# Optimization experiments

Hardware: AMD Instinct MI355X
Metric: run time of the kernel (lower is better)

The kernel has to match this reference:

```python
import jax, jax.numpy as jnp
import numpy as np

B, C, N, K, G = 4, 128, 4096, 9, 4


def setup_inputs() -> dict:
    key = jax.random.key(0)
    ks = jax.random.split(key, 4)
    s = 0.05
    return {
        "features": jax.random.normal(ks[0], (B, C, N, 1), jnp.float32),
        # Attn.linear: Conv2d(2C -> C, 1x1)
        "w_lin": jax.random.normal(ks[1], (C, 2 * C), jnp.float32) * s,
        "b_lin": jnp.zeros((C,), jnp.float32),
        # atten_weight_conv: Linear(C -> K*G)
        "w_aw": jax.random.normal(ks[2], (K * G, C), jnp.float32) * s,
        "b_aw": jnp.zeros((K * G,), jnp.float32),
        # GroupNorm(4, C)
        "gn_g": jnp.ones((C,), jnp.float32),
        "gn_b": jnp.zeros((C,), jnp.float32),
        # conv: Conv2d(C -> C, 1x1) + BatchNorm2d(C)
        "conv_w": jax.random.normal(ks[3], (C, C), jnp.float32) * s,
        "conv_b": jnp.zeros((C,), jnp.float32),
        "bn_g": jnp.ones((C,), jnp.float32),
        "bn_b": jnp.zeros((C,), jnp.float32),
    }


def reference(features, w_lin, b_lin, w_aw, b_aw, gn_g, gn_b, conv_w, conv_b, bn_g, bn_b):
    B, C, N, _ = features.shape
    K, G = 9, 4
    Cg = C // G  # 32 channels per group
    EPS = 1e-5

    x = features[..., 0]                       # [B,C,N]
    # ---- KNN graph (negative squared distance, top-k) ----
    xx = jnp.sum(x * x, axis=1)                # [B,N]
    inner = jnp.einsum('bcn,bcm->bnm', x, x)   # [B,N,N]
    pd = 2.0 * inner - xx[:, :, None] - xx[:, None, :]
    idx = jax.lax.top_k(pd, K)[1]              # [B,N,K]

    # ---- edge feature gather: cat(x, x - x_neighbor) ----
    xt = x.transpose(0, 2, 1)                  # [B,N,C]
    b_ix = jnp.arange(B)[:, None, None]
    nbr = xt[b_ix, idx]                        # [B,N,K,C]
    ctr = jnp.broadcast_to(xt[:, :, None, :], (B, N, K, C))
    edge = jnp.concatenate([ctr, ctr - nbr], axis=-1)   # [B,N,K,2C]

    # ---- Attn.linear (1x1 conv == per-position linear) ----
    feat = jnp.einsum('bnke,ce->bnkc', edge, w_lin) + b_lin  # [B,N,K,C]

    # ---- grouped channel attention (4 groups of 32) ----
    fg = feat.reshape(B, N, K, G, Cg)
    scores = jnp.einsum('bnkgc,bnjgc->bngkj', fg, fg) / np.sqrt(32.0)
    s = jax.nn.softmax(scores, axis=-1)        # [B,N,G,K,K]
    attn = jnp.einsum('bngkj,bnjgc->bngkc', s, jax.nn.elu(fg))  # [B,N,G,K,Cg]

    # ---- attention weights over neighbors ----
    aw = jnp.einsum('bnc,dc->bnd', xt, w_aw) + b_aw          # [B,N,K*G]
    aw = jax.nn.softmax(aw.reshape(B, N, G, K), axis=-1)     # [B,N,G,K]

    # ---- weighted neighbor combine ----
    lf = jnp.einsum('bngk,bngkc->bngc', aw, attn)            # [B,N,G,Cg]
    lf = lf.transpose(0, 2, 3, 1).reshape(B, C, N, 1)        # [B,C,N,1]

    # ---- GroupNorm(4, C) over residual ----
    y = lf + features
    yg = y.reshape(B, G, Cg * N)
    mu = yg.mean(-1, keepdims=True)
    var = yg.var(-1, keepdims=True)
    yn = ((yg - mu) / jnp.sqrt(var + EPS)).reshape(B, C, N, 1)
    yn = yn * gn_g[None, :, None, None] + gn_b[None, :, None, None]

    # ---- 1x1 conv + BatchNorm (training-mode batch stats) + ReLU ----
    z = jnp.einsum('oc,bcnk->bonk', conv_w, yn) + conv_b[None, :, None, None]
    m = z.mean(axis=(0, 2, 3), keepdims=True)
    v = z.var(axis=(0, 2, 3), keepdims=True)
    z = (z - m) / jnp.sqrt(v + EPS) * bn_g[None, :, None, None] + bn_b[None, :, None, None]
    return jax.nn.relu(z)
```

## Files before the change

### kernel.cpp

```cpp
#include <hip/hip_runtime.h>
#include <hip/hip_bf16.h>
#include <cstddef>

#define NPTS 4096
#define CCH  128
#define KNN  9
#define GRP  4
#define BB   4
#define OFF_XT    0u
#define OFF_XX    2097152u
#define OFF_XHI   2113536u
#define OFF_IDX   3162112u
#define OFF_O     3309568u
#define OFF_Y     8159232u
#define OFF_GNP   10256384u
#define OFF_GNA   10387456u
#define OFF_GND   10387968u
#define OFF_WP    10388480u
#define OFF_BIASP 10454016u
#define OFF_BNSUM 10454528u
#define OFF_BNSQ  10454656u
#define OFF_BNSC  10454784u
#define OFF_BNSH  10454912u

using bf16x8 = __attribute__((ext_vector_type(8))) short;
using f32x4  = __attribute__((ext_vector_type(4))) float;

#define CE(a, b) { float _h = fmaxf(a, b); b = fminf(a, b); a = _h; }

#define SENT_BITS 0xFF7FF000u

__global__ void k_transpose(const float* __restrict__ x, float* __restrict__ xt,
                            __hip_bfloat16* __restrict__ xhi, float* __restrict__ xx) {
  __shared__ float t[32][33];
  int tx = threadIdx.x, ty = threadIdx.y;
  int n0 = blockIdx.x * 32, c0 = blockIdx.y * 32, b = blockIdx.z;
  float v = x[((size_t)b * CCH + c0 + ty) * NPTS + n0 + tx];
  t[ty][tx] = v;
  __syncthreads();
  float tv = t[tx][ty];
  size_t R = (size_t)b * NPTS + n0 + ty;
  int c = c0 + tx;
  xt[R * CCH + c] = tv;
  int g = c >> 3, w = c & 7;
  int sc = (((g ^ ((n0 + ty) & 15)) << 3) | w);
  xhi[R * CCH + sc] = __float2bfloat16(tv);
  if (ty == 0) {
    float s = 0.f;
    #pragma unroll
    for (int k = 0; k < 32; k++) { float u = t[k][tx]; s += u * u; }
    atomicAdd(&xx[b * NPTS + n0 + tx], s);
  }
}

__device__ __forceinline__ void select_chunk(int c, int wave, int quad,
                                             const f32x4 (&acc)[2][2],
                                             float (&top8)[2][8]) {
  const unsigned cbase = (unsigned)(c * 128 + wave * 32 + quad * 4);
  #pragma unroll
  for (int qt = 0; qt < 2; qt++) {
    float k[8];
    #pragma unroll
    for (int ct = 0; ct < 2; ct++)
      #pragma unroll
      for (int r = 0; r < 4; r++) {
        unsigned u = __float_as_uint(acc[ct][qt][r]);
        k[ct * 4 + r] = __uint_as_float((u & 0xFFFFF000u) |
                                        (cbase + (unsigned)(ct * 16 + r)));
      }
    CE(k[0],k[1]) CE(k[2],k[3]) CE(k[4],k[5]) CE(k[6],k[7])
    CE(k[0],k[2]) CE(k[1],k[3]) CE(k[4],k[6]) CE(k[5],k[7])
    CE(k[1],k[2]) CE(k[5],k[6])
    CE(k[0],k[4]) CE(k[1],k[5]) CE(k[2],k[6]) CE(k[3],k[7])
    CE(k[2],k[4]) CE(k[3],k[5])
    CE(k[1],k[2]) CE(k[3],k[4]) CE(k[5],k[6])
    float t[8];
    #pragma unroll
    for (int i = 0; i < 8; i++) t[i] = fmaxf(top8[qt][i], k[7 - i]);
    CE(t[0],t[4]) CE(t[1],t[5]) CE(t[2],t[6]) CE(t[3],t[7])
    CE(t[0],t[2]) CE(t[1],t[3]) CE(t[4],t[6]) CE(t[5],t[7])
    CE(t[0],t[1]) CE(t[2],t[3]) CE(t[4],t[5]) CE(t[6],t[7])
    #pragma unroll
    for (int i = 0; i < 8; i++) top8[qt][i] = t[i];
  }
}

__device__ __forceinline__ void load_chunk(const short* __restrict__ xb,
                                           const int (&aoff)[2][4], int c,
                                           bf16x8 (&af)[2][4]) {
  const short* cb = xb + c * (128 * CCH);
  #pragma unroll
  for (int ct = 0; ct < 2; ct++)
    #pragma unroll
    for (int ks = 0; ks < 4; ks++)
      af[ct][ks] = *(const bf16x8*)(cb + aoff[ct][ks]);
}

__launch_bounds__(256, 3)
__global__ void k_knn(const short* __restrict__ xhi, const float* __restrict__ xx,
                      float* __restrict__ cand) {
  __shared__ short Qs[32 * 136];
  __shared__ float XXs[2048];
  const int tid = threadIdx.x;
  const int wave = tid >> 6, lane = tid & 63;
  const int quad = lane >> 4, m = lane & 15;
  const int b = blockIdx.y;
  const int q0 = blockIdx.x * 32;
  const int ch0 = blockIdx.z * 16;
  const short* xb = xhi + (size_t)b * NPTS * CCH;
  const float* xxb = xx + (b << 12);

  {
    int f = tid;
    #pragma unroll
    for (int it = 0; it < 2; it++, f += 256) {
      int row = f >> 4, s = f & 15;
      bf16x8 v = *(const bf16x8*)(xb + (size_t)(q0 + row) * CCH + s * 8);
      int g = s ^ (row & 15);
      *(bf16x8*)&Qs[row * 136 + g * 8] = v;
    }
    const float4* src4 = (const float4*)(xxb + ch0 * 128);
    float4* dst4 = (float4*)XXs;
    #pragma unroll
    for (int j = 0; j < 2; j++) {
      float4 v = src4[tid * 2 + j];
      dst4[tid * 2 + j] = make_float4(-0.5f * v.x, -0.5f * v.y, -0.5f * v.z, -0.5f * v.w);
    }
  }

  int aoff[2][4];
  #pragma unroll
  for (int ct = 0; ct < 2; ct++)
    #pragma unroll
    for (int ks = 0; ks < 4; ks++)
      aoff[ct][ks] = (wave * 32 + ct * 16 + m) * CCH + (((ks * 4 + quad) ^ m) * 8);

  float top8[2][8];
  #pragma unroll
  for (int qt = 0; qt < 2; qt++)
    #pragma unroll
    for (int p = 0; p < 8; p++) top8[qt][p] = __uint_as_float(SENT_BITS);

  f32x4 acc[2][2];
  bf16x8 bufA[2][4], bufB[2][4];

  unsigned qoff = (unsigned)(m * 272 + quad * 16);
  const unsigned xbase = (unsigned)(wave * 128 + quad * 16);

  load_chunk(xb, aoff, ch0, bufA);
  __syncthreads();

  auto mfma_lds = [&](const bf16x8 (&af)[2][4], int crel) {
    unsigned xo = xbase + (unsigned)crel * 512u;
    f32x4 ci0 = *(const f32x4*)((const char*)XXs + xo);
    f32x4 ci1 = *(const f32x4*)((const char*)XXs + xo + 64);
    acc[0][0] = ci0; acc[0][1] = ci0; acc[1][0] = ci1; acc[1][1] = ci1;
    #pragma unroll
    for (int ks = 0; ks < 4; ks++) {
      bf16x8 qv0 = *(const bf16x8*)((const char*)Qs + qoff + ks * 64);
      bf16x8 qv1 = *(const bf16x8*)((const char*)Qs + qoff + 4352 + ks * 64);
      acc[0][0] = __builtin_amdgcn_mfma_f32_16x16x32_bf16(af[0][ks], qv0, acc[0][0], 0, 0, 0);
      acc[0][1] = __builtin_amdgcn_mfma_f32_16x16x32_bf16(af[0][ks], qv1, acc[0][1], 0, 0, 0);
      acc[1][0] = __builtin_amdgcn_mfma_f32_16x16x32_bf16(af[1][ks], qv0, acc[1][0], 0, 0, 0);
      acc[1][1] = __builtin_amdgcn_mfma_f32_16x16x32_bf16(af[1][ks], qv1, acc[1][1], 0, 0, 0);
    }
  };

  for (int c = ch0; c < ch0 + 16; c += 2) {
    load_chunk(xb, aoff, c + 1, bufB);
    if (c > ch0) select_chunk(c - 1, wave, quad, acc, top8);
    asm volatile("" : "+v"(qoff));
    mfma_lds(bufA, c - ch0);
    if (c + 2 < ch0 + 16) load_chunk(xb, aoff, c + 2, bufA);
    select_chunk(c, wave, quad, acc, top8);
    asm volatile("" : "+v"(qoff));
    mfma_lds(bufB, c + 1 - ch0);
  }
  select_chunk(ch0 + 15, wave, quad, acc, top8);

  int slot = wave * 4 + quad;
  #pragma unroll
  for (int qt = 0; qt < 2; qt++) {
    int q = q0 + qt * 16 + m;
    float* dst = cand + ((size_t)((b << 12) + q) * 32 + blockIdx.z * 16 + slot) * 8;
    #pragma unroll
    for (int p = 0; p < 8; p++) dst[p] = top8[qt][p];
  }
}

__launch_bounds__(256)
__global__ void k_rerank(const float* __restrict__ cand, const float* __restrict__ xt,
                         const float* __restrict__ xx, int* __restrict__ idxOut) {
  __shared__ __align__(16) float arr[4][128];
  __shared__ int selS[4][16];
  __shared__ float keyS[4][16];
  int tid = threadIdx.x, wave = tid >> 6, lane = tid & 63;
  int qg = blockIdx.x * 4 + wave;
  int b = qg >> 12;
  const float* src = cand + (size_t)qg * 256;
  if (lane < 16) {
    float4 a0 = *(const float4*)&src[lane * 8];
    float4 a1 = *(const float4*)&src[lane * 8 + 4];
    float4 b0 = *(const float4*)&src[128 + lane * 8];
    float4 b1 = *(const float4*)&src[128 + lane * 8 + 4];
    arr[wave][lane * 8 + 0] = fmaxf(a0.x, b1.w);
    arr[wave][lane * 8 + 1] = fmaxf(a0.y, b1.z);
    arr[wave][lane * 8 + 2] = fmaxf(a0.z, b1.y);
    arr[wave][lane * 8 + 3] = fmaxf(a0.w, b1.x);
    arr[wave][lane * 8 + 4] = fmaxf(a1.x, b0.w);
    arr[wave][lane * 8 + 5] = fmaxf(a1.y, b0.z);
    arr[wave][lane * 8 + 6] = fmaxf(a1.z, b0.y);
    arr[wave][lane * 8 + 7] = fmaxf(a1.w, b0.x);
  }
  __syncthreads();
  float e1 = arr[wave][lane], e2 = arr[wave][lane + 64];
  int r1 = 0, r2 = 0;
  #pragma unroll 8
  for (int f = 0; f < 128; f += 4) {
    float4 fv = *(const float4*)&arr[wave][f];
    r1 += (fv.x > e1) + (fv.y > e1) + (fv.z > e1) + (fv.w > e1);
    r2 += (fv.x > e2) + (fv.y > e2) + (fv.z > e2) + (fv.w > e2);
  }
  if (r1 < 16) selS[wave][r1] = (int)(__float_as_uint(e1) & 0xFFFu);
  if (r2 < 16) selS[wave][r2] = (int)(__float_as_uint(e2) & 0xFFFu);
  __syncthreads();
  int cnum = lane >> 2, part = lane & 3;
  int cidx = selS[wave][cnum];
  const float* rq = xt + (size_t)qg * CCH;
  const float* rc = xt + ((size_t)(b << 12) + cidx) * CCH;
  float dot = 0.f;
  #pragma unroll
  for (int j = 0; j < 8; j++) {
    float4 a4 = *(const float4*)&rq[part * 32 + j * 4];
    float4 c4 = *(const float4*)&rc[part * 32 + j * 4];
    dot += a4.x * c4.x + a4.y * c4.y + a4.z * c4.z + a4.w * c4.w;
  }
  dot += __shfl_xor(dot, 1);
  dot += __shfl_xor(dot, 2);
  if (part == 0)
    keyS[wave][cnum] = fmaf(2.f, dot, -xx[(b << 12) + cidx]);
  __syncthreads();
  if (lane < 16) {
    float k = keyS[wave][lane]; int i = selS[wave][lane];
    int r = 0;
    #pragma unroll
    for (int f = 0; f < 16; f++) {
      float fk = keyS[wave][f]; int fi = selS[wave][f];
      r += (fk > k) || (fk == k && fi < i);
    }
    if (r < 9) idxOut[(size_t)qg * 9 + r] = i;
  }
}

__launch_bounds__(256)
__global__ void k_linear(const float* __restrict__ xt, const float* __restrict__ w_lin,
                         const float* __restrict__ b_lin, const float* __restrict__ w_aw,
                         const float* __restrict__ b_aw, float* __restrict__ O) {
  __shared__ __align__(16) float Xs[64 * 132];
  __shared__ __align__(16) float Ws[64 * 132];
  int tid = threadIdx.x;
  int tx = tid & 15, ty = tid >> 4;
  int p0 = blockIdx.x * 64, o0 = blockIdx.y * 64;
  #pragma unroll
  for (int i = 0; i < 8; i++) {
    int flat = tid + i * 256; int r = flat >> 5, c4 = flat & 31;
    *(float4*)&Xs[r * 132 + c4 * 4] = *(const float4*)&xt[(size_t)(p0 + r) * CCH + c4 * 4];
  }
  #pragma unroll
  for (int i = 0; i < 8; i++) {
    int flat = tid + i * 256; int r = flat >> 5, c4 = flat & 31;
    int o = o0 + r; float4 v;
    if (o < 128) {
      float4 a = *(const float4*)&w_lin[(size_t)o * 256 + c4 * 4];
      float4 c = *(const float4*)&w_lin[(size_t)o * 256 + 128 + c4 * 4];
      v = make_float4(a.x + c.x, a.y + c.y, a.z + c.z, a.w + c.w);
    } else if (o < 256) {
      v = *(const float4*)&w_lin[(size_t)(o - 128) * 256 + 128 + c4 * 4];
    } else if (o < 292) {
      v = *(const float4*)&w_aw[(size_t)(o - 256) * 128 + c4 * 4];
    } else v = make_float4(0.f, 0.f, 0.f, 0.f);
    *(float4*)&Ws[r * 132 + c4 * 4] = v;
  }
  __syncthreads();
  float acc[4][4] = {};
  #pragma unroll 2
  for (int kq = 0; kq < 32; kq++) {
    float4 xa[4], wb[4];
    #pragma unroll
    for (int i = 0; i < 4; i++) xa[i] = *(const float4*)&Xs[(ty * 4 + i) * 132 + kq * 4];
    #pragma unroll
    for (int j = 0; j < 4; j++) wb[j] = *(const float4*)&Ws[(tx + 16 * j) * 132 + kq * 4];
    #pragma unroll
    for (int i = 0; i < 4; i++)
      #pragma unroll
      for (int j = 0; j < 4; j++)
        acc[i][j] += xa[i].x * wb[j].x + xa[i].y * wb[j].y + xa[i].z * wb[j].z + xa[i].w * wb[j].w;
  }
  #pragma unroll
  for (int j = 0; j < 4; j++) {
    int o = o0 + tx + 16 * j;
    if (o < 292) {
      float bias = (o < 128) ? b_lin[o] : ((o < 256) ? 0.f : b_aw[o - 256]);
      #pragma unroll
      for (int i = 0; i < 4; i++)
        O[(size_t)(p0 + ty * 4 + i) * 296 + o] = acc[i][j] + bias;
    }
  }
}

__launch_bounds__(256)
__global__ void k_attn(const float* __restrict__ O, const int* __restrict__ idxArr,
                       const float* __restrict__ xt, float* __restrict__ Y,
                       float* __restrict__ gnPart) {
  __shared__ __align__(16) float fF[4][1188];
  __shared__ __align__(16) float scS[4][432];
  __shared__ float awS[4][48];
  __shared__ float w9S[4][48];
  __shared__ int tI[45], tJ[45];
  int tid = threadIdx.x;
  int wave = tid >> 6, l = tid & 63;
  int pos = blockIdx.x * 4 + wave;
  int b = pos >> 12;
  if (tid == 0) {
    int p = 0;
    for (int i = 0; i < 9; i++) for (int j = i; j < 9; j++) { tI[p] = i; tJ[p] = j; p++; }
  }
  int nbr[9];
  const float* Op = O + (size_t)pos * 296;
  #pragma unroll
  for (int k = 0; k < 9; k++) nbr[k] = idxArr[(size_t)pos * 9 + k];
  float2 u = *(const float2*)(Op + 2 * l);
  float* fFw = fF[wave];
  #pragma unroll
  for (int k = 0; k < 9; k++) {
    const float* vp = O + (size_t)((b << 12) + nbr[k]) * 296 + 128;
    float2 vv = *(const float2*)(vp + 2 * l);
    *(float2*)&fFw[k * 132 + 2 * l] = make_float2(u.x - vv.x, u.y - vv.y);
  }
  __syncthreads();
  #pragma unroll
  for (int r = 0; r < 3; r++) {
    int p = r * 64 + l;
    if (p < 180) {
      int g = p / 45, q = p - g * 45;
      int i = tI[q], j = tJ[q];
      const float* fi = fFw + i * 132 + g * 32;
      const float* fj = fFw + j * 132 + g * 32;
      float s = 0.f;
      #pragma unroll
      for (int t8 = 0; t8 < 8; t8++) {
        float4 a4 = *(const float4*)(fi + 4 * t8);
        float4 b4 = *(const float4*)(fj + 4 * t8);
        s += a4.x * b4.x + a4.y * b4.y + a4.z * b4.z + a4.w * b4.w;
      }
      s *= 0.17677669529663687f;
      scS[wave][(g * 9 + i) * 12 + j] = s;
      scS[wave][(g * 9 + j) * 12 + i] = s;
    }
  }
  __syncthreads();
  if (l < 36) {
    int g = l / 9, i = l - g * 9;
    float* rp = &scS[wave][(g * 9 + i) * 12];
    float mx = rp[0];
    #pragma unroll
    for (int j = 1; j < 9; j++) mx = fmaxf(mx, rp[j]);
    float e[9]; float sm = 0.f;
    #pragma unroll
    for (int j = 0; j < 9; j++) { e[j] = __expf(rp[j] - mx); sm += e[j]; }
    float inv = 1.f / sm;
    #pragma unroll
    for (int j = 0; j < 9; j++) rp[j] = e[j] * inv;
  } else if (l < 40) {
    int g = l - 36;
    float a[9]; float mx = -3.4e38f;
    #pragma unroll
    for (int k = 0; k < 9; k++) { a[k] = Op[256 + g * 9 + k]; mx = fmaxf(mx, a[k]); }
    float sm = 0.f;
    #pragma unroll
    for (int k = 0; k < 9; k++) { a[k] = __expf(a[k] - mx); sm += a[k]; }
    float inv = 1.f / sm;
    #pragma unroll
    for (int k = 0; k < 9; k++) awS[wave][g * 12 + k] = a[k] * inv;
  }
  __syncthreads();
  if (l < 36) {
    int g = l / 9, j = l - g * 9;
    float s = 0.f;
    #pragma unroll
    for (int i = 0; i < 9; i++) s += awS[wave][g * 12 + i] * scS[wave][(g * 9 + i) * 12 + j];
    w9S[wave][g * 12 + j] = s;
  }
  __syncthreads();
  int g = l >> 4;
  float w9r[9];
  #pragma unroll
  for (int j = 0; j < 9; j++) w9r[j] = w9S[wave][g * 12 + j];
  int c0 = 2 * l;
  float lf0 = 0.f, lf1 = 0.f;
  #pragma unroll
  for (int j = 0; j < 9; j++) {
    float2 f2 = *(const float2*)&fFw[j * 132 + c0];
    float e0 = f2.x > 0.f ? f2.x : __expf(f2.x) - 1.f;
    float e1 = f2.y > 0.f ? f2.y : __expf(f2.y) - 1.f;
    lf0 += w9r[j] * e0;
    lf1 += w9r[j] * e1;
  }
  float2 xv = *(const float2*)(xt + (size_t)pos * CCH + c0);
  float y0 = lf0 + xv.x, y1 = lf1 + xv.y;
  *(float2*)(Y + (size_t)pos * CCH + c0) = make_float2(y0, y1);
  float s1 = y0 + y1, s2 = y0 * y0 + y1 * y1;
  #pragma unroll
  for (int mm = 1; mm <= 8; mm <<= 1) { s1 += __shfl_xor(s1, mm); s2 += __shfl_xor(s2, mm); }
  if ((l & 15) == 0) {
    gnPart[(size_t)pos * 8 + g * 2]     = s1;
    gnPart[(size_t)pos * 8 + g * 2 + 1] = s2;
  }
}

__global__ void k_gnstats(const float* __restrict__ gnPart,
                          const float* __restrict__ gn_g, const float* __restrict__ gn_b,
                          float* __restrict__ gnA, float* __restrict__ gnD) {
  int bg = blockIdx.x; int b = bg >> 2, g = bg & 3;
  int tid = threadIdx.x;
  float s1 = 0.f, s2 = 0.f;
  for (int r = tid; r < NPTS; r += 256) {
    const float* p = gnPart + (size_t)(b * NPTS + r) * 8 + g * 2;
    s1 += p[0]; s2 += p[1];
  }
  __shared__ float r1[256], r2[256];
  r1[tid] = s1; r2[tid] = s2;
  __syncthreads();
  for (int off = 128; off > 0; off >>= 1) {
    if (tid < off) { r1[tid] += r1[tid + off]; r2[tid] += r2[tid + off]; }
    __syncthreads();
  }
  __shared__ float muS, rsS;
  if (tid == 0) {
    float mu = r1[0] * (1.f / 131072.f);
    float var = r2[0] * (1.f / 131072.f) - mu * mu;
    muS = mu; rsS = 1.f / sqrtf(var + 1e-5f);
  }
  __syncthreads();
  if (tid < 32) {
    int c = g * 32 + tid;
    float a = rsS * gn_g[c];
    gnA[b * 128 + c] = a;
    gnD[b * 128 + c] = gn_b[c] - muS * a;
  }
}

__global__ void k_fold(const float* __restrict__ conv_w, const float* __restrict__ conv_b,
                       const float* __restrict__ gnA, const float* __restrict__ gnD,
                       float* __restrict__ Wp, float* __restrict__ biasp) {
  int b = blockIdx.x; int tid = threadIdx.x;
  __shared__ float dS[128], aS[128];
  if (tid < 128) { dS[tid] = gnD[b * 128 + tid]; aS[tid] = gnA[b * 128 + tid]; }
  __syncthreads();
  for (int f = tid; f < 16384; f += 256)
    Wp[(size_t)b * 16384 + f] = conv_w[f] * aS[f & 127];
  if (tid < 128) {
    float s = conv_b[tid];
    for (int c = 0; c < 128; c++) s += conv_w[tid * 128 + c] * dS[c];
    biasp[b * 128 + tid] = s;
  }
}

__launch_bounds__(256)
__global__ void k_conv(const float* __restrict__ Y, const float* __restrict__ Wp,
                       const float* __restrict__ biasp, float* __restrict__ zpre,
                       float* __restrict__ bnSum, float* __restrict__ bnSq) {
  __shared__ __align__(16) float Ys[64 * 132];
  __shared__ __align__(16) float Ws[64 * 132];
  int tid = threadIdx.x;
  int tx = tid & 15, ty = tid >> 4;
  int n0 = blockIdx.x * 64, o0 = blockIdx.y * 64, b = blockIdx.z;
  #pragma unroll
  for (int i = 0; i < 8; i++) {
    int flat = tid + i * 256; int r = flat >> 5, c4 = flat & 31;
    *(float4*)&Ys[r * 132 + c4 * 4] = *(const float4*)&Y[(size_t)((b << 12) + n0 + r) * CCH + c4 * 4];
    *(float4*)&Ws[r * 132 + c4 * 4] = *(const float4*)&Wp[(size_t)b * 16384 + (size_t)(o0 + r) * 128 + c4 * 4];
  }
  __syncthreads();
  float acc[4][4] = {};
  #pragma unroll 2
  for (int kq = 0; kq < 32; kq++) {
    float4 wa[4], yb[4];
    #pragma unroll
    for (int i = 0; i < 4; i++) wa[i] = *(const float4*)&Ws[(ty * 4 + i) * 132 + kq * 4];
    #pragma unroll
    for (int j = 0; j < 4; j++) yb[j] = *(const float4*)&Ys[(tx + 16 * j) * 132 + kq * 4];
    #pragma unroll
    for (int i = 0; i < 4; i++)
      #pragma unroll
      for (int j = 0; j < 4; j++)
        acc[i][j] += wa[i].x * yb[j].x + wa[i].y * yb[j].y + wa[i].z * yb[j].z + wa[i].w * yb[j].w;
  }
  #pragma unroll
  for (int i = 0; i < 4; i++) {
    int o = o0 + ty * 4 + i;
    float bias = biasp[b * 128 + o];
    float p1 = 0.f, p2 = 0.f;
    #pragma unroll
    for (int j = 0; j < 4; j++) {
      float z = acc[i][j] + bias;
      zpre[(((size_t)((b << 7) + o)) << 12) + n0 + tx + 16 * j] = z;
      p1 += z; p2 += z * z;
    }
    #pragma unroll
    for (int mm = 1; mm <= 8; mm <<= 1) { p1 += __shfl_xor(p1, mm); p2 += __shfl_xor(p2, mm); }
    if (tx == 0) { atomicAdd(&bnSum[o], p1); atomicAdd(&bnSq[o], p2); }
  }
}

__global__ void k_bnfin(const float* __restrict__ bnSum, const float* __restrict__ bnSq,
                        const float* __restrict__ bn_g, const float* __restrict__ bn_b,
                        float* __restrict__ bnScale, float* __restrict__ bnShift) {
  int o = threadIdx.x;
  float m = bnSum[o] * (1.f / 16384.f);
  float v = bnSq[o] * (1.f / 16384.f) - m * m;
  float sc = bn_g[o] / sqrtf(v + 1e-5f);
  bnScale[o] = sc;
  bnShift[o] = bn_b[o] - m * sc;
}

__global__ void k_final(const float* __restrict__ zpre, const float* __restrict__ bnScale,
                        const float* __restrict__ bnShift, float* __restrict__ out) {
  int i4 = blockIdx.x * 256 + threadIdx.x;
  int e = i4 * 4;
  int o = (e >> 12) & 127;
  float4 z = *(const float4*)&zpre[e];
  float sc = bnScale[o], sh = bnShift[o];
  float4 r;
  r.x = fmaxf(fmaf(z.x, sc, sh), 0.f);
  r.y = fmaxf(fmaf(z.y, sc, sh), 0.f);
  r.z = fmaxf(fmaf(z.z, sc, sh), 0.f);
  r.w = fmaxf(fmaf(z.w, sc, sh), 0.f);
  *(float4*)&out[e] = r;
}

extern "C" void kernel_launch(void* const* d_in, const int* in_sizes, int n_in,
                              void* d_out, int out_size, void* d_ws, size_t ws_size,
                              hipStream_t stream) {
  const float* features = (const float*)d_in[0];
  const float* w_lin  = (const float*)d_in[1];
  const float* b_lin  = (const float*)d_in[2];
  const float* w_aw   = (const float*)d_in[3];
  const float* b_aw   = (const float*)d_in[4];
  const float* gn_g   = (const float*)d_in[5];
  const float* gn_b   = (const float*)d_in[6];
  const float* conv_w = (const float*)d_in[7];
  const float* conv_b = (const float*)d_in[8];
  const float* bn_g   = (const float*)d_in[9];
  const float* bn_b   = (const float*)d_in[10];

  float* ws    = (float*)d_ws;
  float* xt    = ws + OFF_XT;
  float* xxp   = ws + OFF_XX;
  __hip_bfloat16* xhip = (__hip_bfloat16*)(ws + OFF_XHI);
  int*   idxp  = (int*)(ws + OFF_IDX);
  float* Op    = ws + OFF_O;
  float* candp = ws + OFF_O;
  float* Yp    = ws + OFF_Y;
  float* gnp   = ws + OFF_GNP;
  float* gnA   = ws + OFF_GNA;
  float* gnD   = ws + OFF_GND;
  float* Wp    = ws + OFF_WP;
  float* biasp = ws + OFF_BIASP;
  float* bnSum = ws + OFF_BNSUM;
  float* bnSq  = ws + OFF_BNSQ;
  float* bnSc  = ws + OFF_BNSC;
  float* bnSh  = ws + OFF_BNSH;
  float* zpre  = xt;

  hipMemsetAsync(xxp, 0, NPTS * BB * sizeof(float), stream);
  hipMemsetAsync(bnSum, 0, 256 * sizeof(float), stream);

  k_transpose<<<dim3(128, 4, 4), dim3(32, 32), 0, stream>>>(features, xt, xhip, xxp);
  k_knn<<<dim3(128, 4, 2), 256, 0, stream>>>((const short*)xhip, xxp, candp);
  k_rerank<<<4096, 256, 0, stream>>>(candp, xt, xxp, idxp);
  k_linear<<<dim3(256, 5), 256, 0, stream>>>(xt, w_lin, b_lin, w_aw, b_aw, Op);
  k_attn<<<4096, 256, 0, stream>>>(Op, idxp, xt, Yp, gnp);
  k_gnstats<<<16, 256, 0, stream>>>(gnp, gn_g, gn_b, gnA, gnD);
  k_fold<<<4, 256, 0, stream>>>(conv_w, conv_b, gnA, gnD, Wp, biasp);
  k_conv<<<dim3(64, 2, 4), 256, 0, stream>>>(Yp, Wp, biasp, zpre, bnSum, bnSq);
  k_bnfin<<<1, 128, 0, stream>>>(bnSum, bnSq, bn_g, bn_b, bnSc, bnSh);
  k_final<<<2048, 256, 0, stream>>>(zpre, bnSc, bnSh, (float*)d_out);
}
```

Measured before the change: 270.6 us.

## Split KNN candidate search into three column chunks to raise occupancy

The KNN kernel's key-column range is now split across three z-blocks of 11/11/10 chunks instead of two blocks of 16, which adds more workgroups. An odd-count tail path is added to the double-buffered loop. The rerank kernel now merges three sorted candidate lists: it max-merges the first two bitonically, sorts the result, then max-merges with the third. The goal is better GPU fill on the dominant KNN stage, at the cost of larger candidate buffers and a bit more merge work in rerank.

```diff
diff --git a/kernel.cpp b/kernel.cpp
--- a/kernel.cpp
+++ b/kernel.cpp
@@ -100,13 +100,15 @@
 __global__ void k_knn(const short* __restrict__ xhi, const float* __restrict__ xx,
                       float* __restrict__ cand) {
   __shared__ short Qs[32 * 136];
-  __shared__ float XXs[2048];
+  __shared__ float XXs[1408];
   const int tid = threadIdx.x;
   const int wave = tid >> 6, lane = tid & 63;
   const int quad = lane >> 4, m = lane & 15;
   const int b = blockIdx.y;
   const int q0 = blockIdx.x * 32;
-  const int ch0 = blockIdx.z * 16;
+  const int z = blockIdx.z;
+  const int ch0 = z * 11;
+  const int cnt = (z == 2) ? 10 : 11;
   const short* xb = xhi + (size_t)b * NPTS * CCH;
   const float* xxb = xx + (b << 12);
 
@@ -121,10 +123,10 @@
     }
     const float4* src4 = (const float4*)(xxb + ch0 * 128);
     float4* dst4 = (float4*)XXs;
-    #pragma unroll
-    for (int j = 0; j < 2; j++) {
-      float4 v = src4[tid * 2 + j];
-      dst4[tid * 2 + j] = make_float4(-0.5f * v.x, -0.5f * v.y, -0.5f * v.z, -0.5f * v.w);
+    int nf4 = cnt * 32;
+    for (int i = tid; i < nf4; i += 256) {
+      float4 v = src4[i];
+      dst4[i] = make_float4(-0.5f * v.x, -0.5f * v.y, -0.5f * v.z, -0.5f * v.w);
     }
   }
 
@@ -166,23 +168,29 @@
     }
   };
 
-  for (int c = ch0; c < ch0 + 16; c += 2) {
+  int c = ch0;
+  for (; c + 1 < ch0 + cnt; c += 2) {
     load_chunk(xb, aoff, c + 1, bufB);
     if (c > ch0) select_chunk(c - 1, wave, quad, acc, top8);
     asm volatile("" : "+v"(qoff));
     mfma_lds(bufA, c - ch0);
-    if (c + 2 < ch0 + 16) load_chunk(xb, aoff, c + 2, bufA);
+    if (c + 2 < ch0 + cnt) load_chunk(xb, aoff, c + 2, bufA);
     select_chunk(c, wave, quad, acc, top8);
     asm volatile("" : "+v"(qoff));
     mfma_lds(bufB, c + 1 - ch0);
   }
-  select_chunk(ch0 + 15, wave, quad, acc, top8);
+  if (cnt & 1) {
+    select_chunk(ch0 + cnt - 2, wave, quad, acc, top8);
+    asm volatile("" : "+v"(qoff));
+    mfma_lds(bufA, cnt - 1);
+  }
+  select_chunk(ch0 + cnt - 1, wave, quad, acc, top8);
 
   int slot = wave * 4 + quad;
   #pragma unroll
   for (int qt = 0; qt < 2; qt++) {
     int q = q0 + qt * 16 + m;
-    float* dst = cand + ((size_t)((b << 12) + q) * 32 + blockIdx.z * 16 + slot) * 8;
+    float* dst = cand + ((size_t)((b << 12) + q) * 48 + z * 16 + slot) * 8;
     #pragma unroll
     for (int p = 0; p < 8; p++) dst[p] = top8[qt][p];
   }
@@ -197,20 +205,28 @@
   int tid = threadIdx.x, wave = tid >> 6, lane = tid & 63;
   int qg = blockIdx.x * 4 + wave;
   int b = qg >> 12;
-  const float* src = cand + (size_t)qg * 256;
+  const float* src = cand + (size_t)qg * 384;
   if (lane < 16) {
-    float4 a0 = *(const float4*)&src[lane * 8];
-    float4 a1 = *(const float4*)&src[lane * 8 + 4];
-    float4 b0 = *(const float4*)&src[128 + lane * 8];
-    float4 b1 = *(const float4*)&src[128 + lane * 8 + 4];
-    arr[wave][lane * 8 + 0] = fmaxf(a0.x, b1.w);
-    arr[wave][lane * 8 + 1] = fmaxf(a0.y, b1.z);
-    arr[wave][lane * 8 + 2] = fmaxf(a0.z, b1.y);
-    arr[wave][lane * 8 + 3] = fmaxf(a0.w, b1.x);
-    arr[wave][lane * 8 + 4] = fmaxf(a1.x, b0.w);
-    arr[wave][lane * 8 + 5] = fmaxf(a1.y, b0.z);
-    arr[wave][lane * 8 + 6] = fmaxf(a1.z, b0.y);
-    arr[wave][lane * 8 + 7] = fmaxf(a1.w, b0.x);
+    const float* pa = src + lane * 8;
+    float4 a0 = *(const float4*)pa,         a1 = *(const float4*)(pa + 4);
+    float4 b0 = *(const float4*)(pa + 128), b1 = *(const float4*)(pa + 132);
+    float4 c0 = *(const float4*)(pa + 256), c1 = *(const float4*)(pa + 260);
+    float t[8];
+    t[0] = fmaxf(a0.x, b1.w); t[1] = fmaxf(a0.y, b1.z);
+    t[2] = fmaxf(a0.z, b1.y); t[3] = fmaxf(a0.w, b1.x);
+    t[4] = fmaxf(a1.x, b0.w); t[5] = fmaxf(a1.y, b0.z);
+    t[6] = fmaxf(a1.z, b0.y); t[7] = fmaxf(a1.w, b0.x);
+    CE(t[0],t[4]) CE(t[1],t[5]) CE(t[2],t[6]) CE(t[3],t[7])
+    CE(t[0],t[2]) CE(t[1],t[3]) CE(t[4],t[6]) CE(t[5],t[7])
+    CE(t[0],t[1]) CE(t[2],t[3]) CE(t[4],t[5]) CE(t[6],t[7])
+    arr[wave][lane * 8 + 0] = fmaxf(t[0], c1.w);
+    arr[wave][lane * 8 + 1] = fmaxf(t[1], c1.z);
+    arr[wave][lane * 8 + 2] = fmaxf(t[2], c1.y);
+    arr[wave][lane * 8 + 3] = fmaxf(t[3], c1.x);
+    arr[wave][lane * 8 + 4] = fmaxf(t[4], c0.w);
+    arr[wave][lane * 8 + 5] = fmaxf(t[5], c0.z);
+    arr[wave][lane * 8 + 6] = fmaxf(t[6], c0.y);
+    arr[wave][lane * 8 + 7] = fmaxf(t[7], c0.x);
   }
   __syncthreads();
   float e1 = arr[wave][lane], e2 = arr[wave][lane + 64];
@@ -577,7 +593,7 @@
   hipMemsetAsync(bnSum, 0, 256 * sizeof(float), stream);
 
   k_transpose<<<dim3(128, 4, 4), dim3(32, 32), 0, stream>>>(features, xt, xhip, xxp);
-  k_knn<<<dim3(128, 4, 2), 256, 0, stream>>>((const short*)xhip, xxp, candp);
+  k_knn<<<dim3(128, 4, 3), 256, 0, stream>>>((const short*)xhip, xxp, candp);
   k_rerank<<<4096, 256, 0, stream>>>(candp, xt, xxp, idxp);
   k_linear<<<dim3(256, 5), 256, 0, stream>>>(xt, w_lin, b_lin, w_aw, b_aw, Op);
   k_attn<<<4096, 256, 0, stream>>>(Op, idxp, xt, Yp, gnp);
```

Result: no change. 271.3 us (+0.3%).
